# Kernel tuning notes

Measured on AMD Instinct MI355X. Metric: run time of the kernel, lower is better.

Reference implementation:

```python
import jax, jax.numpy as jnp
import numpy as np
from functools import reduce

# 6x6 open-boundary PEPS, bond dim D=4, physical dim 2, boundary contraction
# from ymin with projector compression to CHI=8, projectors perturbed by a
# 2-layer MLP of the spin configuration (eta = 1e-3), then full contraction.
Lx, Ly, D, PHYS = 6, 6, 4, 2
CHI = 8
NHID = 64
ETA = 1e-3
NSITES = Lx * Ly
BATCH = 1024


def _proj_shapes():
    # Static propagation of projector tensor shapes (mirrors the sweep below).
    u = [1] + [D] * (Lx - 1)
    d = [D] * (Lx - 1) + [1]
    shapes = []
    for j in range(1, Ly - 1):
        nu = [u[i] * (1 if i == 0 else D) for i in range(Lx)]
        nd = [d[i] * (1 if i == Lx - 1 else D) for i in range(Lx)]
        for i in range(Lx - 1):
            m = nd[i]
            k1 = min(nu[i] * D, m)
            k2 = min(D * nd[i + 1], m)
            cb = min(CHI, k1, k2)
            shapes += [(m, cb), (m, cb)]
            nd[i] = cb
            nu[i + 1] = cb
        u, d = nu, nd
    return shapes


PROJ_SHAPES = _proj_shapes()
PROJ_LEN = sum(m * c for m, c in PROJ_SHAPES)  # == 6400


def _site(T, xi, i, j):
    # select physical index; axes of result: (up, right, down, left)
    t = jnp.take(T[i, j], xi[i * Ly + j], axis=-1)
    if i == 0:
        t = t[:1]          # lattice top edge: up bond is trivial
    if i == Lx - 1:
        t = t[:, :, :1]    # lattice bottom edge: down bond is trivial
    return t


def _sweep(A, projs):
    # boundary MPS from column 0; B[i] axes: (u, r, d)
    B = [A[i][0][:, :, :, 0] for i in range(Lx)]
    out = [] if projs is None else None
    p = 0
    for j in range(1, Ly - 1):
        Bn = []
        for i in range(Lx):
            t = A[i][j]  # (a, R, b, l)
            nt = jnp.einsum('uxd,aRbx->uaRdb', B[i], t)
            u_, a_, R_, d_, b_ = nt.shape
            Bn.append(nt.reshape(u_ * a_, R_, d_ * b_))
        for i in range(Lx - 1):
            Tt, Tb = Bn[i], Bn[i + 1]
            m = Tt.shape[-1]
            if projs is None:
                mt = Tt.reshape(-1, m)        # (ut*R, m)
                mb = Tb.reshape(m, -1)        # (m, R*db)
                R1 = jnp.linalg.qr(mt, mode='r')     # (k1, m)
                R2 = jnp.linalg.qr(mb.T, mode='r')   # (k2, m)
                U, S, Vh = jnp.linalg.svd(R1 @ R2.T, full_matrices=False)
                cb = min(CHI, S.shape[-1])
                sinv = 1.0 / jnp.sqrt(S[:cb] + 1e-12)
                Pd = (R2.T @ Vh[:cb].T) * sinv  # (m, cb): top tensor's down bond
                Pu = (R1.T @ U[:, :cb]) * sinv  # (m, cb): bottom tensor's up bond
                out += [Pd, Pu]
            else:
                Pd, Pu = projs[p], projs[p + 1]
                p += 2
            Bn[i] = jnp.einsum('uRm,mc->uRc', Tt, Pd)
            Bn[i + 1] = jnp.einsum('mRd,mc->cRd', Tb, Pu)
        B = Bn
    return B, out


def _finalize(B, A):
    Cs = []
    for i in range(Lx):
        t = A[i][Ly - 1][:, 0]  # (a, b, l): right bond is trivial
        c = jnp.einsum('uxd,abx->uadb', B[i], t)
        ua, aa, dd, bb = c.shape
        Cs.append(c.reshape(ua * aa, dd * bb))
    return reduce(jnp.matmul, Cs)[0, 0]


def _mlp(xf, W1, b1, W2, b2):
    h = jax.nn.relu(xf @ W1.T + b1)
    return h @ W2.T + b2


def _amp_single(T, W1, b1, W2, b2, xi):
    A = [[_site(T, xi, i, j) for j in range(Ly)] for i in range(Lx)]
    # pass 1: compute data-dependent projectors
    _, plist = _sweep(A, None)
    vec = jnp.concatenate([pp.reshape(-1) for pp in plist])
    vec = vec + _mlp(xi.astype(jnp.float32), W1, b1, W2, b2) * ETA
    # unpack perturbed projectors
    newp, ptr = [], 0
    for pp in plist:
        n = pp.size
        newp.append(vec[ptr:ptr + n].reshape(pp.shape))
        ptr += n
    # pass 2: contract the full network with the perturbed projectors
    B, _ = _sweep(A, newp)
    return _finalize(B, A)


def setup_inputs() -> dict:
    key = jax.random.key(0)
    ks = jax.random.split(key, 6)
    T = jax.random.normal(ks[0], (Lx, Ly, D, D, D, D, PHYS), dtype=jnp.float32) * 0.5
    W1 = jax.random.normal(ks[1], (NHID, NSITES), dtype=jnp.float32) / np.sqrt(NSITES).astype(np.float32)
    b1 = jnp.zeros((NHID,), dtype=jnp.float32)
    W2 = jax.random.normal(ks[2], (PROJ_LEN, NHID), dtype=jnp.float32) / np.sqrt(NHID).astype(np.float32)
    b2 = jnp.zeros((PROJ_LEN,), dtype=jnp.float32)
    x = jax.random.randint(ks[3], (BATCH, NSITES), 0, PHYS, dtype=jnp.int32)
    return {"T": T, "W1": W1, "b1": b1, "W2": W2, "b2": b2, "x": x}


def reference(T, W1, b1, W2, b2, x):
    return jax.vmap(lambda xi: _amp_single(T, W1, b1, W2, b2, xi))(x)
```

## Files before the change

### kernel.cpp

```cpp
#include <hip/hip_runtime.h>

__device__ const int g_uprev[2][6] = {{1,4,4,4,4,4},{1,4,8,8,8,4}};
__device__ const int g_dprev[2][6] = {{4,4,4,4,4,1},{4,8,8,8,4,1}};
__device__ const int g_mtab[2][5]  = {{16,16,16,16,16},{16,32,32,32,16}};
__device__ const int g_cbtab[5]    = {4,8,8,8,4};
__device__ const int g_ucurtab[5]  = {1,4,8,8,8};
__device__ const int g_dntab[2][5] = {{16,16,16,16,1},{32,32,32,16,1}};
__device__ const int g_path[2][5]  = {{0,0,1,1,2},{0,0,0,0,2}};
__device__ const int g_offtab[4][5]= {{0,128,384,640,896},
                                      {1024,1152,1664,2176,2688},
                                      {2816,2944,3456,3968,4480},
                                      {4608,4736,5248,5760,6272}};
__device__ const int g_ufin[6] = {1,4,8,8,8,4};
__device__ const int g_dfin[6] = {4,8,8,8,4,1};

__global__ __launch_bounds__(256) void mlp_kernel(
    const float* __restrict__ W1, const float* __restrict__ b1,
    const float* __restrict__ W2, const float* __restrict__ b2,
    const int* __restrict__ x, float* __restrict__ proj)
{
  __shared__ float hbuf[8][64];
  const int tid = threadIdx.x;
  const int s0 = blockIdx.x << 3;
  for (int e = tid; e < 512; e += 256) {
    const int sl = e >> 6, hh = e & 63;
    const int* xr = x + (s0 + sl) * 36;
    const float* wr = W1 + hh * 36;
    float acc = b1[hh];
    #pragma unroll
    for (int t = 0; t < 36; ++t) acc += wr[t] * (float)xr[t];
    hbuf[sl][hh] = fmaxf(acc, 0.0f);
  }
  __syncthreads();
  for (int k = tid; k < 6400; k += 256) {
    const float4* wr = (const float4*)(W2 + (size_t)k * 64);
    float acc[8];
    #pragma unroll
    for (int s2 = 0; s2 < 8; ++s2) acc[s2] = 0.0f;
    #pragma unroll
    for (int c = 0; c < 16; ++c) {
      const float4 w = wr[c];
      #pragma unroll
      for (int s2 = 0; s2 < 8; ++s2) {
        const float4 hv = ((const float4*)hbuf[s2])[c];
        acc[s2] += w.x * hv.x + w.y * hv.y + w.z * hv.z + w.w * hv.w;
      }
    }
    const float bb = b2[k];
    #pragma unroll
    for (int s2 = 0; s2 < 8; ++s2)
      proj[(size_t)(s0 + s2) * 6400 + k] = 0.001f * (acc[s2] + bb);
  }
}

__device__ __forceinline__ void jrot(float app, float aqq, float apq, float& c, float& sn) {
  c = 1.0f; sn = 0.0f;
  if (fabsf(apq) > 1e-36f + 1e-12f * (fabsf(app) + fabsf(aqq))) {
    const float tau = (aqq - app) * 0.5f * __builtin_amdgcn_rcpf(apq);
    const float t = copysignf(1.0f, tau) *
                    __builtin_amdgcn_rcpf(fabsf(tau) + __builtin_amdgcn_sqrtf(1.0f + tau * tau));
    c = __builtin_amdgcn_rsqf(1.0f + t * t);
    sn = t * c;
  }
}

template<int N>
__device__ void jacobi_pb(float* __restrict__ H, float* __restrict__ V, int tid)
{
  constexpr int NP = N / 2;
  constexpr int NM1 = N - 1;
  constexpr int NL = (N == 32) ? 5 : ((N == 16) ? 4 : 2);
  constexpr int NBMAX = (N == 32) ? 2 : 1;
  constexpr int NVMAX = (N == 32) ? 4 : 1;
  constexpr int MAXSW = (N == 32) ? 5 : ((N == 16) ? 5 : 3);
  for (int e = tid; e < N * N; e += 128) {
    const int r = e >> NL, c = e & (N - 1);
    V[r * 36 + c] = (r == c) ? 1.0f : 0.0f;
  }
  __syncthreads();
  const int cp = tid & (NP - 1);
  const bool hact = (N == 32) ? true : (tid < NP * NP);
  const bool vact = (N >= 16) ? true : (tid < N * NP);
  int ca  = (cp == 0) ? NM1 : cp;
  int cb2 = (cp == 0) ? 0 : (NM1 - cp);
  int ra[NBMAX], rb[NBMAX], rt[NBMAX];
  #pragma unroll
  for (int bi = 0; bi < NBMAX; ++bi) {
    const int t = (N == 32) ? ((tid >> 4) + 8 * bi) : ((N == 16) ? (tid >> 3) : (tid >> 1));
    rt[bi] = t;
    const int tm = t % NM1;
    ra[bi] = (t == 0) ? NM1 : tm;
    rb[bi] = (t == 0) ? 0 : (NM1 - tm) % NM1;
  }
  for (int sw = 0; sw < MAXSW; ++sw) {
    for (int rd = 0; rd < NM1; ++rd) {
      const int q0 = (ca < cb2) ? ca : cb2;
      const int q1 = (ca < cb2) ? cb2 : ca;
      float cc_, cs_;
      jrot(H[q0 * 37], H[q1 * 37], H[q0 * 36 + q1], cc_, cs_);
      float o00[NBMAX], o01[NBMAX], o10[NBMAX], o11[NBMAX];
      int P0[NBMAX], P1[NBMAX];
      #pragma unroll
      for (int bi = 0; bi < NBMAX; ++bi) {
        if (bi == 0 && !hact) continue;
        const int p0 = (ra[bi] < rb[bi]) ? ra[bi] : rb[bi];
        const int p1 = (ra[bi] < rb[bi]) ? rb[bi] : ra[bi];
        const float cr_ = __shfl(cc_, rt[bi]);
        const float sr_ = __shfl(cs_, rt[bi]);
        const float a  = H[p0 * 36 + q0], b = H[p0 * 36 + q1];
        const float c2 = H[p1 * 36 + q0], d = H[p1 * 36 + q1];
        const float t1 = cr_ * a - sr_ * c2, t2 = cr_ * b - sr_ * d;
        const float u1 = sr_ * a + cr_ * c2, u2 = sr_ * b + cr_ * d;
        o00[bi] = cc_ * t1 - cs_ * t2; o01[bi] = cs_ * t1 + cc_ * t2;
        o10[bi] = cc_ * u1 - cs_ * u2; o11[bi] = cs_ * u1 + cc_ * u2;
        P0[bi] = p0; P1[bi] = p1;
      }
      float v0[NVMAX], v1[NVMAX];
      #pragma unroll
      for (int vi = 0; vi < NVMAX; ++vi) {
        if (vi == 0 && !vact) continue;
        const int row = (N == 32) ? ((tid >> 4) + 8 * vi) : ((N == 16) ? (tid >> 3) : (tid >> 1));
        const float a0 = V[row * 36 + q0], a1 = V[row * 36 + q1];
        v0[vi] = cc_ * a0 - cs_ * a1; v1[vi] = cs_ * a0 + cc_ * a1;
      }
      __syncthreads();
      #pragma unroll
      for (int bi = 0; bi < NBMAX; ++bi) {
        if (bi == 0 && !hact) continue;
        H[P0[bi] * 36 + q0] = o00[bi]; H[P0[bi] * 36 + q1] = o01[bi];
        H[P1[bi] * 36 + q0] = o10[bi]; H[P1[bi] * 36 + q1] = o11[bi];
      }
      #pragma unroll
      for (int vi = 0; vi < NVMAX; ++vi) {
        if (vi == 0 && !vact) continue;
        const int row = (N == 32) ? ((tid >> 4) + 8 * vi) : ((N == 16) ? (tid >> 3) : (tid >> 1));
        V[row * 36 + q0] = v0[vi]; V[row * 36 + q1] = v1[vi];
      }
      __syncthreads();
      ca  = (cp == 0) ? NM1 : ((ca + 1 == NM1) ? 0 : ca + 1);
      cb2 = (cb2 + 1 == NM1) ? 0 : cb2 + 1;
      #pragma unroll
      for (int bi = 0; bi < NBMAX; ++bi) {
        ra[bi] = (rt[bi] == 0) ? NM1 : ((ra[bi] + 1 == NM1) ? 0 : ra[bi] + 1);
        rb[bi] = (rb[bi] + 1 == NM1) ? 0 : rb[bi] + 1;
      }
    }
  }
}

__device__ __forceinline__ void gram_cols(float* __restrict__ G, const float* __restrict__ A,
                                          int nrows, int mcols, bool init, int tid)
{
  const int q4 = mcols >> 2;
  const int q4log = (mcols == 32) ? 3 : 2;
  const int nel = mcols * q4;
  const float4* A4 = (const float4*)A;
  float4* G4 = (float4*)G;
  for (int e = tid; e < nel; e += 128) {
    const int c2q = e & (q4 - 1);
    const int c1 = e >> q4log;
    float ax = 0.f, ay = 0.f, az = 0.f, aw = 0.f;
    for (int r = 0; r < nrows; ++r) {
      const float a1 = A[r * 36 + c1];
      const float4 a2 = A4[r * 9 + c2q];
      ax += a1 * a2.x; ay += a1 * a2.y; az += a1 * a2.z; aw += a1 * a2.w;
    }
    float4* gp = G4 + c1 * 9 + c2q;
    if (init) { float4 o; o.x = ax; o.y = ay; o.z = az; o.w = aw; *gp = o; }
    else { float4 o = *gp; o.x += ax; o.y += ay; o.z += az; o.w += aw; *gp = o; }
  }
  __syncthreads();
}

__device__ __forceinline__ void absorb_T(const float* __restrict__ Tg, const float* __restrict__ poolS,
    float* __restrict__ BIGT, float* __restrict__ ATile, const int* __restrict__ xi,
    int i1, int j, int U, int Dd, int rr0, int rr1, int tid)
{
  const int bd = (i1 == 5) ? 1 : 4;
  const int dbw = Dd * bd;
  const int mt_ = U * 4;
  const int ph = xi[i1 * 6 + j];
  const float* tb = Tg + (size_t)(i1 * 6 + j) * 512;
  for (int e = tid; e < 256; e += 128) ATile[e] = tb[e * 2 + ph];
  __syncthreads();
  const int mlog = (mt_ == 32) ? 5 : 4;
  const int dblog = 31 - __clz(dbw);
  const int bdlog = (bd == 4) ? 2 : 0;
  const int nel = mt_ * dbw * (rr1 - rr0);
  for (int e = tid; e < nel; e += 128) {
    const int ua = e & (mt_ - 1);
    const int db = (e >> mlog) & (dbw - 1);
    const int rr = rr0 + (e >> (mlog + dblog));
    const int u = ua >> 2, a = ua & 3;
    const int d_ = db >> bdlog, b = db & (bd - 1);
    const float* op = poolS + u * 33 + d_;
    const float4 av = *(const float4*)(ATile + a * 64 + rr * 16 + b * 4);
    BIGT[((rr - rr0) * dbw + db) * 36 + ua] = op[0] * av.x + op[8] * av.y + op[16] * av.z + op[24] * av.w;
  }
  __syncthreads();
}

__global__ __launch_bounds__(128, 2) void peps_kernel(
    const float* __restrict__ Tg, const int* __restrict__ x,
    float* __restrict__ proj, float* __restrict__ out)
{
  __shared__ float pool[6 * 264];
  __shared__ float CUR[1152];
  __shared__ float BIGT[2304];
  __shared__ float GbM[1152];
  __shared__ float TM[1152];
  __shared__ float GM[1152];
  __shared__ float ATile[256];
  __shared__ float PdL[256], PuL[256];
  __shared__ float red[4];
  __shared__ int isel[8];
  __shared__ float sinvv[8], sdiv[8];
  __shared__ int xi[36];
  __shared__ float vvec[36], vvec2[36];

  const int s = blockIdx.x;
  const int tid = threadIdx.x;
  if (tid < 36) xi[tid] = x[s * 36 + tid];
  __syncthreads();

  for (int sweep = 0; sweep < 2; ++sweep) {
    for (int i2 = 0; i2 < 6; ++i2) {
      const int ad = (i2 == 0) ? 1 : 4, bd = (i2 == 5) ? 1 : 4;
      const int bdlog = (bd == 4) ? 2 : 0;
      const int ph = xi[i2 * 6];
      const float* tb = Tg + (size_t)(i2 * 6) * 512;
      const int nel = ad * 4 * bd;
      for (int e = tid; e < nel; e += 128) {
        const int b = e & (bd - 1);
        const int rr = (e >> bdlog) & 3;
        const int a = e >> (bdlog + 2);
        pool[i2 * 264 + a * 33 + rr * 8 + b] = tb[(a * 64 + rr * 16 + b * 4) * 2 + ph];
      }
    }
    __syncthreads();

    for (int j = 1; j <= 4; ++j) {
      const int jj = (j > 1) ? 1 : 0;
      {
        const int ph = xi[j];
        const float* tb = Tg + (size_t)j * 512;
        for (int e = tid; e < 256; e += 128) ATile[e] = tb[e * 2 + ph];
        __syncthreads();
        for (int e = tid; e < 64; e += 128) {
          const int db = e & 15;
          const int rr = e >> 4;
          const int d_ = db >> 2, b = db & 3;
          const float* op = pool + d_;
          const float4 av = *(const float4*)(ATile + rr * 16 + b * 4);
          CUR[rr * 36 + db] = op[0] * av.x + op[8] * av.y + op[16] * av.z + op[24] * av.w;
        }
        __syncthreads();
      }

      for (int i = 0; i < 5; ++i) {
        const int m = g_mtab[jj][i], cb = g_cbtab[i], ucur = g_ucurtab[i], dn = g_dntab[jj][i];
        const int p = ucur * 4, path = g_path[jj][i];
        const int U1 = g_uprev[jj][i + 1], Dd1 = g_dprev[jj][i + 1];
        const bool two = (dn == 32);
        const int cblog = (cb == 8) ? 3 : 2;
        const int mq4 = m >> 2;
        float* projb = proj + (size_t)s * 6400 + g_offtab[j - 1][i];

        if (sweep == 0) {
          if (path == 2) {
            absorb_T(Tg, pool + (i + 1) * 264, BIGT, ATile, xi, i + 1, j, U1, Dd1, 0, 4, tid);
            gram_cols(GbM, CUR, p, m, true, tid);
            for (int e = tid; e < 64; e += 128) {
              const int r = e & 3, k = e >> 2;
              float acc = 0.f;
              const float4* G4 = (const float4*)GbM;
              const float4* B4 = (const float4*)BIGT;
              for (int lq = 0; lq < 4; ++lq) {
                const float4 g = G4[k * 9 + lq], b = B4[r * 9 + lq];
                acc += g.x * b.x + g.y * b.y + g.z * b.z + g.w * b.w;
              }
              TM[k * 36 + r] = acc;
            }
            __syncthreads();
            for (int e = tid; e < 16; e += 128) {
              const int c = e & 3, r = e >> 2;
              float acc = 0.f;
              for (int k = 0; k < 16; ++k) acc += BIGT[r * 36 + k] * TM[k * 36 + c];
              GM[r * 36 + c] = acc;
            }
            __syncthreads();
            jacobi_pb<4>(GM, TM + 576, tid);
          } else if (path == 0) {
            if (!two) {
              absorb_T(Tg, pool + (i + 1) * 264, BIGT, ATile, xi, i + 1, j, U1, Dd1, 0, 4, tid);
              gram_cols(GbM, BIGT, 4 * dn, m, true, tid);
            } else {
              absorb_T(Tg, pool + (i + 1) * 264, BIGT, ATile, xi, i + 1, j, U1, Dd1, 0, 2, tid);
              gram_cols(GbM, BIGT, 2 * dn, m, true, tid);
              absorb_T(Tg, pool + (i + 1) * 264, BIGT, ATile, xi, i + 1, j, U1, Dd1, 2, 4, tid);
              gram_cols(GbM, BIGT, 2 * dn, m, false, tid);
            }
            const int q4log = (m == 32) ? 3 : 2;
            for (int e = tid; e < p * mq4; e += 128) {
              const int lq = e & (mq4 - 1), pr = e >> q4log;
              float ax = 0.f, ay = 0.f, az = 0.f, aw = 0.f;
              const float4* G4 = (const float4*)GbM;
              for (int k = 0; k < m; ++k) {
                const float a1 = CUR[pr * 36 + k];
                const float4 g = G4[k * 9 + lq];
                ax += a1 * g.x; ay += a1 * g.y; az += a1 * g.z; aw += a1 * g.w;
              }
              float4 o; o.x = ax; o.y = ay; o.z = az; o.w = aw;
              ((float4*)TM)[pr * 9 + lq] = o;
            }
            __syncthreads();
            const int plog = (p == 32) ? 5 : ((p == 16) ? 4 : 2);
            for (int e = tid; e < p * p; e += 128) {
              const int pc = e & (p - 1), pr = e >> plog;
              float acc = 0.f;
              const float4* T4 = (const float4*)TM;
              const float4* C4 = (const float4*)CUR;
              for (int lq = 0; lq < mq4; ++lq) {
                const float4 t = T4[pr * 9 + lq], c = C4[pc * 9 + lq];
                acc += t.x * c.x + t.y * c.y + t.z * c.z + t.w * c.w;
              }
              GM[pr * 36 + pc] = acc;
            }
            __syncthreads();
            if (p == 4)       jacobi_pb<4>(GM, TM, tid);
            else if (p == 16) jacobi_pb<16>(GM, TM, tid);
            else              jacobi_pb<32>(GM, TM, tid);
          } else {
            absorb_T(Tg, pool + (i + 1) * 264, BIGT, ATile, xi, i + 1, j, U1, Dd1, 0, 4, tid);
            gram_cols(GbM + 576, CUR, p, m, true, tid);
            gram_cols(GbM, BIGT, 4 * dn, m, true, tid);
            if (tid < 64) {
              float v_ = (tid < 16) ? GbM[tid * 37] : -3.0e38f;
              for (int mk = 32; mk; mk >>= 1) v_ = fmaxf(v_, __shfl_xor(v_, mk));
              if (tid == 0) red[0] = v_;
            }
            __syncthreads();
            const float thr = 1e-10f * red[0] + 1e-35f;
            for (int k = 0; k < 16; ++k) {
              const float dk = GbM[k * 37];
              const float rs = (dk > thr) ? (1.0f / sqrtf(dk)) : 0.0f;
              if (tid < 16) TM[k * 36 + tid] = GbM[k * 36 + tid] * rs;
              __syncthreads();
              const int rows = 15 - k;
              for (int e = tid; e < rows * 16; e += 128) {
                const int ii = k + 1 + (e >> 4), jc = e & 15;
                GbM[ii * 36 + jc] -= TM[k * 36 + ii] * TM[k * 36 + jc];
              }
              __syncthreads();
            }
            for (int e = tid; e < 64; e += 128) {
              const int jq = e & 3, k = e >> 2;
              float ax = 0.f, ay = 0.f, az = 0.f, aw = 0.f;
              const float4* Gt4 = (const float4*)(GbM + 576);
              for (int l = 0; l < 16; ++l) {
                const float r2 = TM[k * 36 + l];
                const float4 g = Gt4[l * 9 + jq];
                ax += r2 * g.x; ay += r2 * g.y; az += r2 * g.z; aw += r2 * g.w;
              }
              float4 o; o.x = ax; o.y = ay; o.z = az; o.w = aw;
              ((float4*)(TM + 576))[k * 9 + jq] = o;
            }
            __syncthreads();
            for (int e = tid; e < 256; e += 128) {
              const int k2 = e & 15, k = e >> 4;
              float acc = 0.f;
              const float4* T14 = (const float4*)(TM + 576);
              const float4* R24 = (const float4*)TM;
              for (int lq = 0; lq < 4; ++lq) {
                const float4 t = T14[k * 9 + lq], r = R24[k2 * 9 + lq];
                acc += t.x * r.x + t.y * r.y + t.z * r.z + t.w * r.w;
              }
              GM[k * 36 + k2] = acc;
            }
            __syncthreads();
            jacobi_pb<16>(GM, TM + 576, tid);
          }

          const int N = (path == 2) ? 4 : ((path == 1) ? 16 : p);
          if (tid < 64) {
            float v_ = (tid < N) ? GM[tid * 37] : -3.0e38f;
            int ix = tid;
            for (int t = 0; t < cb; ++t) {
              float bv = v_; int bi = ix;
              for (int mk = 32; mk; mk >>= 1) {
                const float ov = __shfl_xor(bv, mk);
                const int oi = __shfl_xor(bi, mk);
                if (ov > bv || (ov == bv && oi < bi)) { bv = ov; bi = oi; }
              }
              if (tid == 0) isel[t] = bi;
              if (ix == bi) v_ = -3.0e38f;
            }
          }
          __syncthreads();
          if (tid < cb) {
            const float lam = GM[isel[tid] * 37];
            const float s_ = sqrtf(fmaxf(lam, 0.0f));
            sinvv[tid] = 1.0f / sqrtf(s_ + 1e-12f);
            sdiv[tid]  = 1.0f / fmaxf(s_, 1e-25f);
          }
          __syncthreads();

          if (path == 0) {
            for (int e = tid; e < m * cb; e += 128) {
              const int k = e & (cb - 1), mrow = e >> cblog;
              const int a = isel[k];
              float acc = 0.f;
              for (int pr = 0; pr < p; ++pr) acc += CUR[pr * 36 + mrow] * TM[pr * 36 + a];
              PuL[mrow * 8 + k] = acc * sinvv[k];
            }
            __syncthreads();
            for (int e = tid; e < m * cb; e += 128) {
              const int k = e & (cb - 1), mrow = e >> cblog;
              float acc = 0.f;
              for (int l = 0; l < m; ++l) acc += GbM[mrow * 36 + l] * PuL[l * 8 + k];
              PdL[mrow * 8 + k] = acc * sdiv[k];
            }
            __syncthreads();
          } else if (path == 2) {
            for (int e = tid; e < m * cb; e += 128) {
              const int k = e & (cb - 1), mrow = e >> cblog;
              const int a = isel[k];
              float acc = 0.f;
              for (int r = 0; r < 4; ++r) acc += BIGT[r * 36 + mrow] * TM[576 + r * 36 + a];
              PdL[mrow * 8 + k] = acc * sinvv[k];
            }
            __syncthreads();
            for (int e = tid; e < m * cb; e += 128) {
              const int k = e & (cb - 1), mrow = e >> cblog;
              float acc = 0.f;
              for (int l = 0; l < m; ++l) acc += GbM[mrow * 36 + l] * PdL[l * 8 + k];
              PuL[mrow * 8 + k] = acc * sdiv[k];
            }
            __syncthreads();
          } else {
            for (int e = tid; e < m * cb; e += 128) {
              const int k = e & (cb - 1), mrow = e >> cblog;
              const int a = isel[k];
              float acc = 0.f;
              for (int t = 0; t < 16; ++t) acc += TM[t * 36 + mrow] * TM[576 + t * 36 + a];
              PdL[mrow * 8 + k] = acc * sinvv[k];
            }
            __syncthreads();
            for (int e = tid; e < m * cb; e += 128) {
              const int k = e & (cb - 1), mrow = e >> cblog;
              float acc = 0.f;
              for (int l = 0; l < m; ++l) acc += GbM[576 + mrow * 36 + l] * PdL[l * 8 + k];
              PuL[mrow * 8 + k] = acc * sdiv[k];
            }
            __syncthreads();
          }
          for (int e = tid; e < m * cb; e += 128)
            projb[e] += PdL[(e >> cblog) * 8 + (e & (cb - 1))];
          for (int e = tid; e < m * cb; e += 128)
            projb[m * cb + e] += PuL[(e >> cblog) * 8 + (e & (cb - 1))];
        } else {
          for (int e = tid; e < m * cb; e += 128)
            PdL[(e >> cblog) * 8 + (e & (cb - 1))] = projb[e];
          for (int e = tid; e < m * cb; e += 128)
            PuL[(e >> cblog) * 8 + (e & (cb - 1))] = projb[m * cb + e];
          __syncthreads();
          if (!two) absorb_T(Tg, pool + (i + 1) * 264, BIGT, ATile, xi, i + 1, j, U1, Dd1, 0, 4, tid);
          else      absorb_T(Tg, pool + (i + 1) * 264, BIGT, ATile, xi, i + 1, j, U1, Dd1, 2, 4, tid);
        }

        {
          const int nel = ucur * 4 * cb;
          const float4* C4 = (const float4*)CUR;
          for (int e = tid; e < nel; e += 128) {
            const int cc = e & (cb - 1);
            const int rr = (e >> cblog) & 3;
            const int u = e >> (cblog + 2);
            const int row = u * 4 + rr;
            float acc = 0.f;
            for (int mq = 0; mq < mq4; ++mq) {
              const float4 cv = C4[row * 9 + mq];
              acc += cv.x * PdL[(mq * 4 + 0) * 8 + cc] + cv.y * PdL[(mq * 4 + 1) * 8 + cc]
                   + cv.z * PdL[(mq * 4 + 2) * 8 + cc] + cv.w * PdL[(mq * 4 + 3) * 8 + cc];
            }
            pool[i * 264 + u * 33 + rr * 8 + cc] = acc;
          }
          __syncthreads();

          const int dnlog = 31 - __clz(dn);
          auto bn1 = [&](int rr0, int nloc) {
            const int ne2 = cb * nloc * dn;
            const float4* B4 = (const float4*)BIGT;
            for (int e = tid; e < ne2; e += 128) {
              const int dd = e & (dn - 1);
              const int t = e >> dnlog;
              const int rrL = t & (nloc - 1);
              const int cc = t >> ((nloc == 4) ? 2 : 1);
              const int row = rrL * dn + dd;
              float acc = 0.f;
              for (int mq = 0; mq < mq4; ++mq) {
                const float4 bv = B4[row * 9 + mq];
                acc += bv.x * PuL[(mq * 4 + 0) * 8 + cc] + bv.y * PuL[(mq * 4 + 1) * 8 + cc]
                     + bv.z * PuL[(mq * 4 + 2) * 8 + cc] + bv.w * PuL[(mq * 4 + 3) * 8 + cc];
              }
              if (i < 4) CUR[(cc * 4 + rr0 + rrL) * 36 + dd] = acc;
              else       pool[5 * 264 + cc * 33 + (rr0 + rrL) * 8] = acc;
            }
            __syncthreads();
          };
          if (!two) {
            bn1(0, 4);
          } else {
            bn1(2, 2);
            absorb_T(Tg, pool + (i + 1) * 264, BIGT, ATile, xi, i + 1, j, U1, Dd1, 0, 2, tid);
            bn1(0, 2);
          }
        }
      }
    }

    if (sweep == 1) {
      if (tid == 0) vvec[0] = 1.0f;
      __syncthreads();
      for (int i = 0; i < 6; ++i) {
        const int ad = (i == 0) ? 1 : 4, bd = (i == 5) ? 1 : 4;
        const int adlog = (ad == 4) ? 2 : 0, bdlog = (bd == 4) ? 2 : 0;
        const int rows = g_ufin[i] * ad, cols = g_dfin[i] * bd;
        const int clog = 31 - __clz(cols);
        const int ph = xi[i * 6 + 5];
        const float* tb = Tg + (size_t)(i * 6 + 5) * 512;
        for (int e = tid; e < 256; e += 128) ATile[e] = tb[e * 2 + ph];
        __syncthreads();
        for (int e = tid; e < rows * cols; e += 128) {
          const int col = e & (cols - 1);
          const int ua = e >> clog;
          const int u = ua >> adlog, a = ua & (ad - 1);
          const int d_ = col >> bdlog, b = col & (bd - 1);
          const float* fb = pool + i * 264 + u * 33 + d_;
          const float4 av = *(const float4*)(ATile + a * 64 + b * 4);
          GM[ua * 36 + col] = fb[0] * av.x + fb[8] * av.y + fb[16] * av.z + fb[24] * av.w;
        }
        __syncthreads();
        if (tid < cols) {
          float acc = 0.f;
          for (int r_ = 0; r_ < rows; ++r_) acc += vvec[r_] * GM[r_ * 36 + tid];
          vvec2[tid] = acc;
        }
        __syncthreads();
        if (tid < cols) vvec[tid] = vvec2[tid];
        __syncthreads();
      }
      if (tid == 0) out[s] = vvec[0];
    }
  }
}

extern "C" void kernel_launch(void* const* d_in, const int* in_sizes, int n_in,
                              void* d_out, int out_size, void* d_ws, size_t ws_size,
                              hipStream_t stream) {
  const float* Tg = (const float*)d_in[0];
  const float* W1 = (const float*)d_in[1];
  const float* b1 = (const float*)d_in[2];
  const float* W2 = (const float*)d_in[3];
  const float* b2 = (const float*)d_in[4];
  const int*   x  = (const int*)d_in[5];
  float* out = (float*)d_out;
  float* proj = (float*)d_ws;
  (void)in_sizes; (void)n_in; (void)out_size; (void)ws_size;

  mlp_kernel<<<dim3(128), dim3(256), 0, stream>>>(W1, b1, W2, b2, x, proj);
  peps_kernel<<<dim3(1024), dim3(128), 0, stream>>>(Tg, x, proj, out);
}
```

Baseline: 1.612 ms.

## Store Jacobi matrix in rotating-seat order so each pair is adjacent

The parallel Jacobi eigen-solver now keeps the Gram matrix and eigenvector columns permuted into a round-robin 'seat' order. Each thread's pivot pair sits in two adjacent columns, so reads become float2 loads and the per-round index rotation bookkeeping goes away. After each rotation, results are written to the shifted seat positions. The Gram-building loops scatter into seat order, and the eigenvector identity initialisation is permuted to match. This cuts LDS instructions and index arithmetic in the inner loop. The risk is that the permuted eigenvector and eigenvalue ordering must stay consistent with the downstream selection code.

Result: faster. 1.497 ms (-7.1%).

```diff
diff --git a/kernel.cpp b/kernel.cpp
--- a/kernel.cpp
+++ b/kernel.cpp
@@ -64,6 +64,16 @@
   }
 }
 
+__device__ __forceinline__ int seatof(int i, int n) {
+  return (i == n - 1) ? 0 : ((i == 0) ? 1 : ((i < (n >> 1)) ? (2 * i) : (2 * (n - 1 - i) + 1)));
+}
+
+__device__ __forceinline__ int sgshift(int s, int np) {
+  if (s == 0) return 0;
+  if (s & 1) return (s == 2 * np - 1) ? (2 * np - 2) : (s + 2);
+  return (s == 2) ? 1 : (s - 2);
+}
+
 template<int N>
 __device__ void jacobi_pb(float* __restrict__ H, float* __restrict__ V, int tid)
 {
@@ -75,75 +85,68 @@
   constexpr int MAXSW = (N == 32) ? 5 : ((N == 16) ? 5 : 3);
   for (int e = tid; e < N * N; e += 128) {
     const int r = e >> NL, c = e & (N - 1);
-    V[r * 36 + c] = (r == c) ? 1.0f : 0.0f;
+    const int i0 = (c == 0) ? NM1 : ((c == 1) ? 0 : ((c & 1) ? (NM1 - (c >> 1)) : (c >> 1)));
+    V[r * 36 + c] = (r == i0) ? 1.0f : 0.0f;
   }
   __syncthreads();
   const int cp = tid & (NP - 1);
   const bool hact = (N == 32) ? true : (tid < NP * NP);
   const bool vact = (N >= 16) ? true : (tid < N * NP);
-  int ca  = (cp == 0) ? NM1 : cp;
-  int cb2 = (cp == 0) ? 0 : (NM1 - cp);
-  int ra[NBMAX], rb[NBMAX], rt[NBMAX];
+  const int q0 = 2 * cp, q1 = q0 + 1;
+  const int d0 = sgshift(q0, NP), d1 = sgshift(q1, NP);
+  int rt[NBMAX], r0[NBMAX], r1[NBMAX], e0[NBMAX], e1[NBMAX];
   #pragma unroll
   for (int bi = 0; bi < NBMAX; ++bi) {
-    const int t = (N == 32) ? ((tid >> 4) + 8 * bi) : ((N == 16) ? (tid >> 3) : (tid >> 1));
-    rt[bi] = t;
-    const int tm = t % NM1;
-    ra[bi] = (t == 0) ? NM1 : tm;
-    rb[bi] = (t == 0) ? 0 : (NM1 - tm) % NM1;
-  }
+    rt[bi] = (N == 32) ? ((tid >> 4) + 8 * bi) : ((N == 16) ? (tid >> 3) : (tid >> 1));
+    r0[bi] = 2 * rt[bi]; r1[bi] = r0[bi] + 1;
+    e0[bi] = sgshift(r0[bi], NP); e1[bi] = sgshift(r1[bi], NP);
+  }
+  int vr[NVMAX];
+  #pragma unroll
+  for (int vi = 0; vi < NVMAX; ++vi)
+    vr[vi] = (N == 32) ? ((tid >> 4) + 8 * vi) : ((N == 16) ? (tid >> 3) : (tid >> 1));
+
   for (int sw = 0; sw < MAXSW; ++sw) {
     for (int rd = 0; rd < NM1; ++rd) {
-      const int q0 = (ca < cb2) ? ca : cb2;
-      const int q1 = (ca < cb2) ? cb2 : ca;
+      const float2 dg = *(const float2*)(H + q0 * 36 + q0);
+      const float aqq = H[q1 * 36 + q1];
       float cc_, cs_;
-      jrot(H[q0 * 37], H[q1 * 37], H[q0 * 36 + q1], cc_, cs_);
+      jrot(dg.x, aqq, dg.y, cc_, cs_);
       float o00[NBMAX], o01[NBMAX], o10[NBMAX], o11[NBMAX];
-      int P0[NBMAX], P1[NBMAX];
       #pragma unroll
       for (int bi = 0; bi < NBMAX; ++bi) {
         if (bi == 0 && !hact) continue;
-        const int p0 = (ra[bi] < rb[bi]) ? ra[bi] : rb[bi];
-        const int p1 = (ra[bi] < rb[bi]) ? rb[bi] : ra[bi];
         const float cr_ = __shfl(cc_, rt[bi]);
         const float sr_ = __shfl(cs_, rt[bi]);
-        const float a  = H[p0 * 36 + q0], b = H[p0 * 36 + q1];
-        const float c2 = H[p1 * 36 + q0], d = H[p1 * 36 + q1];
-        const float t1 = cr_ * a - sr_ * c2, t2 = cr_ * b - sr_ * d;
-        const float u1 = sr_ * a + cr_ * c2, u2 = sr_ * b + cr_ * d;
+        const float2 rA = *(const float2*)(H + r0[bi] * 36 + q0);
+        const float2 rB = *(const float2*)(H + r1[bi] * 36 + q0);
+        const float t1 = cr_ * rA.x - sr_ * rB.x, t2 = cr_ * rA.y - sr_ * rB.y;
+        const float u1 = sr_ * rA.x + cr_ * rB.x, u2 = sr_ * rA.y + cr_ * rB.y;
         o00[bi] = cc_ * t1 - cs_ * t2; o01[bi] = cs_ * t1 + cc_ * t2;
         o10[bi] = cc_ * u1 - cs_ * u2; o11[bi] = cs_ * u1 + cc_ * u2;
-        P0[bi] = p0; P1[bi] = p1;
       }
       float v0[NVMAX], v1[NVMAX];
       #pragma unroll
       for (int vi = 0; vi < NVMAX; ++vi) {
         if (vi == 0 && !vact) continue;
-        const int row = (N == 32) ? ((tid >> 4) + 8 * vi) : ((N == 16) ? (tid >> 3) : (tid >> 1));
-        const float a0 = V[row * 36 + q0], a1 = V[row * 36 + q1];
-        v0[vi] = cc_ * a0 - cs_ * a1; v1[vi] = cs_ * a0 + cc_ * a1;
+        const float2 vv = *(const float2*)(V + vr[vi] * 36 + q0);
+        v0[vi] = cc_ * vv.x - cs_ * vv.y;
+        v1[vi] = cs_ * vv.x + cc_ * vv.y;
       }
       __syncthreads();
       #pragma unroll
       for (int bi = 0; bi < NBMAX; ++bi) {
         if (bi == 0 && !hact) continue;
-        H[P0[bi] * 36 + q0] = o00[bi]; H[P0[bi] * 36 + q1] = o01[bi];
-        H[P1[bi] * 36 + q0] = o10[bi]; H[P1[bi] * 36 + q1] = o11[bi];
+        H[e0[bi] * 36 + d0] = o00[bi]; H[e0[bi] * 36 + d1] = o01[bi];
+        H[e1[bi] * 36 + d0] = o10[bi]; H[e1[bi] * 36 + d1] = o11[bi];
       }
       #pragma unroll
       for (int vi = 0; vi < NVMAX; ++vi) {
         if (vi == 0 && !vact) continue;
-        const int row = (N == 32) ? ((tid >> 4) + 8 * vi) : ((N == 16) ? (tid >> 3) : (tid >> 1));
-        V[row * 36 + q0] = v0[vi]; V[row * 36 + q1] = v1[vi];
+        V[vr[vi] * 36 + d0] = v0[vi];
+        V[vr[vi] * 36 + d1] = v1[vi];
       }
       __syncthreads();
-      ca  = (cp == 0) ? NM1 : ((ca + 1 == NM1) ? 0 : ca + 1);
-      cb2 = (cb2 + 1 == NM1) ? 0 : cb2 + 1;
-      #pragma unroll
-      for (int bi = 0; bi < NBMAX; ++bi) {
-        ra[bi] = (rt[bi] == 0) ? NM1 : ((ra[bi] + 1 == NM1) ? 0 : ra[bi] + 1);
-        rb[bi] = (rb[bi] + 1 == NM1) ? 0 : rb[bi] + 1;
-      }
     }
   }
 }
@@ -204,14 +207,14 @@
     const float* __restrict__ Tg, const int* __restrict__ x,
     float* __restrict__ proj, float* __restrict__ out)
 {
-  __shared__ float pool[6 * 264];
-  __shared__ float CUR[1152];
-  __shared__ float BIGT[2304];
-  __shared__ float GbM[1152];
-  __shared__ float TM[1152];
-  __shared__ float GM[1152];
-  __shared__ float ATile[256];
-  __shared__ float PdL[256], PuL[256];
+  __shared__ __align__(16) float pool[6 * 264];
+  __shared__ __align__(16) float CUR[1152];
+  __shared__ __align__(16) float BIGT[2304];
+  __shared__ __align__(16) float GbM[1152];
+  __shared__ __align__(16) float TM[1152];
+  __shared__ __align__(16) float GM[1152];
+  __shared__ __align__(16) float ATile[256];
+  __shared__ __align__(16) float PdL[256], PuL[256];
   __shared__ float red[4];
   __shared__ int isel[8];
   __shared__ float sinvv[8], sdiv[8];
@@ -286,7 +289,7 @@
               const int c = e & 3, r = e >> 2;
               float acc = 0.f;
               for (int k = 0; k < 16; ++k) acc += BIGT[r * 36 + k] * TM[k * 36 + c];
-              GM[r * 36 + c] = acc;
+              GM[seatof(r, 4) * 36 + seatof(c, 4)] = acc;
             }
             __syncthreads();
             jacobi_pb<4>(GM, TM + 576, tid);
@@ -324,7 +327,7 @@
                 const float4 t = T4[pr * 9 + lq], c = C4[pc * 9 + lq];
                 acc += t.x * c.x + t.y * c.y + t.z * c.z + t.w * c.w;
               }
-              GM[pr * 36 + pc] = acc;
+              GM[seatof(pr, p) * 36 + seatof(pc, p)] = acc;
             }
             __syncthreads();
             if (p == 4)       jacobi_pb<4>(GM, TM, tid);
@@ -375,7 +378,7 @@
                 const float4 t = T14[k * 9 + lq], r = R24[k2 * 9 + lq];
                 acc += t.x * r.x + t.y * r.y + t.z * r.z + t.w * r.w;
               }
-              GM[k * 36 + k2] = acc;
+              GM[seatof(k, 16) * 36 + seatof(k2, 16)] = acc;
             }
             __syncthreads();
             jacobi_pb<16>(GM, TM + 576, tid);
```
